# Kernel tuning notes

Measured on AMD Instinct MI355X. Metric: run time of the kernel, lower is better.

The kernel has to match this reference:

```python
import jax, jax.numpy as jnp
import numpy as np

B, T, C = 4, 2048, 1024
N_HEAD = 16


def setup_inputs() -> dict:
    key = jax.random.key(0)
    k1, k2, k3, k4, k5 = jax.random.split(key, 5)
    x = jax.random.normal(k1, (B, T, C), dtype=jnp.float32)
    # c_attn: Dense(3*C) -> kernel [C, 3C], bias [3C]
    w_attn = jax.random.normal(k2, (C, 3 * C), dtype=jnp.float32) * 0.02
    b_attn = jnp.zeros((3 * C,), dtype=jnp.float32)
    # c_proj: Dense(C) with scaled init 0.02/sqrt(2*n_layer), n_layer=24
    w_proj = jax.random.normal(k3, (C, C), dtype=jnp.float32) * (0.02 / np.sqrt(2 * 24))
    b_proj = jnp.zeros((C,), dtype=jnp.float32)
    return {"x": x, "w_attn": w_attn, "b_attn": b_attn, "w_proj": w_proj, "b_proj": b_proj}


def reference(x, w_attn, b_attn, w_proj, b_proj):
    Bx, Tx, Cx = x.shape
    hd = Cx // N_HEAD  # head dim
    qkv = x @ w_attn + b_attn                      # [B, T, 3C]
    q, k, v = jnp.split(qkv, 3, axis=2)
    q = q.reshape(Bx, Tx, N_HEAD, hd).transpose(0, 2, 1, 3)  # [B, H, T, hd]
    k = k.reshape(Bx, Tx, N_HEAD, hd).transpose(0, 2, 1, 3)
    v = v.reshape(Bx, Tx, N_HEAD, hd).transpose(0, 2, 1, 3)
    mask = jnp.tril(jnp.ones((1, 1, Tx, Tx), dtype=bool))
    att = jnp.einsum('bhqd,bhkd->bhqk', q, k) / jnp.sqrt(jnp.float32(hd))
    att = jnp.where(mask, att, jnp.finfo(jnp.float32).min)
    att = jax.nn.softmax(att, axis=-1)
    y = jnp.einsum('bhqk,bhkd->bhqd', att, v)      # [B, H, T, hd]
    y = y.transpose(0, 2, 1, 3).reshape(Bx, Tx, Cx)
    return y @ w_proj + b_proj
```

## Files before the change

### kernel.cpp

```cpp
#include <hip/hip_runtime.h>
#include <cstdint>
#include <cstddef>

typedef unsigned short u16;
typedef __bf16 bf16_t;
typedef bf16_t bf16x8 __attribute__((ext_vector_type(8)));
typedef float f32x4 __attribute__((ext_vector_type(4)));
typedef float f32x16 __attribute__((ext_vector_type(16)));

__device__ __forceinline__ u16 f32_to_bf16(float f) {
  uint32_t u = __builtin_bit_cast(uint32_t, f);
  u += 0x7fffu + ((u >> 16) & 1u);
  return (u16)(u >> 16);
}

__device__ __forceinline__ uint32_t pack_bf16x2(float lo, float hi) {
  uint32_t a = __builtin_bit_cast(uint32_t, hi) + 0x8000u;
  uint32_t b = __builtin_bit_cast(uint32_t, lo) + 0x8000u;
  return __builtin_amdgcn_perm(a, b, 0x07060302u);
}

__device__ __forceinline__ void gload_lds16(const void* g, void* l) {
  __builtin_amdgcn_global_load_lds(
      (const __attribute__((address_space(1))) unsigned int*)g,
      (__attribute__((address_space(3))) unsigned int*)l, 16, 0, 0);
}

__global__ void cvt_bf16(const float* __restrict__ in, u16* __restrict__ out, int n) {
  int i = (blockIdx.x * 256 + threadIdx.x) * 4;
  if (i < n) {
    float4 f = *(const float4*)(in + i);
    ushort4 o;
    o.x = f32_to_bf16(f.x); o.y = f32_to_bf16(f.y);
    o.z = f32_to_bf16(f.z); o.w = f32_to_bf16(f.w);
    *(ushort4*)(out + i) = o;
  }
}

__global__ void tconv(const float* __restrict__ in, u16* __restrict__ out, int R, int C) {
  __shared__ u16 t[64][80];
  int tid = threadIdx.x;
  int cb = blockIdx.x * 64, rb = blockIdx.y * 64;
  int rr = tid >> 2, cg = (tid & 3) * 16;
  const float* ip = in + (size_t)(rb + rr) * C + cb + cg;
#pragma unroll
  for (int i = 0; i < 16; ++i) t[rr][cg + i] = f32_to_bf16(ip[i]);
  __syncthreads();
  int cc = tid >> 2, rg = (tid & 3) * 16;
  u16* op = out + (size_t)(cb + cc) * R + rb + rg;
  union { uint4 v[2]; u16 s[16]; } tmp;
#pragma unroll
  for (int i = 0; i < 16; ++i) tmp.s[i] = t[rg + i][cc];
  *(uint4*)op = tmp.v[0];
  *(uint4*)(op + 8) = tmp.v[1];
}

__global__ void vtrans(const u16* __restrict__ qkvb, u16* __restrict__ vt) {
  __shared__ u16 t[64][80];
  int tid = threadIdx.x;
  int bh = blockIdx.x, tb = blockIdx.y * 64;
  int b = bh >> 4, h = bh & 15;
  int tt = tid >> 2, dg = (tid & 3) * 16;
  const u16* ip = qkvb + (size_t)(b * 2048 + tb + tt) * 3072 + 2048 + h * 64 + dg;
  union { uint4 v; u16 s[8]; } a0, a1;
  a0.v = *(const uint4*)ip;
  a1.v = *(const uint4*)(ip + 8);
#pragma unroll
  for (int i = 0; i < 8; ++i) { t[tt][dg + i] = a0.s[i]; t[tt][dg + 8 + i] = a1.s[i]; }
  __syncthreads();
  int dd = tid >> 2, tg = (tid & 3) * 16;
  u16* op = vt + (size_t)(bh * 64 + dd) * 2048 + tb + tg;
  union { uint4 v[2]; u16 s[16]; } tmp;
#pragma unroll
  for (int i = 0; i < 16; ++i) {
    int pi = (i & 3) | ((i & 4) << 1) | ((i & 8) >> 1);
    tmp.s[i] = t[tg + pi][dd];
  }
  *(uint4*)op = tmp.v[0];
  *(uint4*)(op + 8) = tmp.v[1];
}

template <int OUT_BF16>
__global__ __launch_bounds__(512, 2) void gemm256(const u16* __restrict__ A,
                                                  const u16* __restrict__ Bt,
                                                  const float* __restrict__ bias,
                                                  void* __restrict__ Cout,
                                                  int M, int N, int K) {
  __shared__ __align__(16) u16 lds[2][2][16384];
  const int tid = threadIdx.x;
  const int w = tid >> 6, L = tid & 63;
  const int quad = L >> 4, lc = L & 15;
  const int wr = w >> 2, wc = w & 3;
  const int wrM = wr * 128, wcN = wc * 64;
  const int rL = L >> 3;
  const int gsw = (L & 7) ^ rL;

  const int nbx = N >> 8;
  const int cpx = gridDim.x >> 3;
  const int id = blockIdx.x;
  const int swz = (id & 7) * cpx + (id >> 3);
  const int tileN = (swz % nbx) << 8;
  const int tileM = (swz / nbx) << 8;
  const int nkt = K >> 6;

  u16* const A0 = &lds[0][0][0];
  u16* const B0 = &lds[0][1][0];
  u16* const A1 = &lds[1][0][0];
  u16* const B1 = &lds[1][1][0];

  auto stageQ = [&](const u16* Mp, int gRow, int kt, u16* reg) {
    int ktc = kt < nkt ? kt : nkt - 1;
    const u16* src = Mp + (size_t)(gRow + w * 8 + rL) * K + (ktc << 6) + gsw * 8;
    gload_lds16(src, reg + w * 512);
  };

  f32x4 acc[8][4] = {};
  const int rsw = lc & 7;
  const int g0 = (quad ^ rsw) * 8;
  const int g1 = ((4 + quad) ^ rsw) * 8;
  const int aRow = (wrM + lc) * 64;
  const int bRow = (wcN + lc) * 64;

  stageQ(A, tileM + 0, 0, A0 + 0);
  stageQ(A, tileM + 128, 0, A0 + 8192);
  stageQ(Bt, tileN + 0, 0, B0 + 0);
  stageQ(Bt, tileN + 64, 0, B0 + 4096);
  stageQ(A, tileM + 64, 0, A0 + 4096);
  stageQ(A, tileM + 192, 0, A0 + 12288);
  stageQ(Bt, tileN + 128, 0, B0 + 8192);
  stageQ(Bt, tileN + 192, 0, B0 + 12288);
  stageQ(A, tileM + 0, 1, A1 + 0);
  stageQ(A, tileM + 128, 1, A1 + 8192);
  stageQ(Bt, tileN + 0, 1, B1 + 0);
  stageQ(Bt, tileN + 64, 1, B1 + 4096);
  stageQ(A, tileM + 64, 1, A1 + 4096);
  stageQ(A, tileM + 192, 1, A1 + 12288);
  asm volatile("s_waitcnt vmcnt(6)" ::: "memory");
  __builtin_amdgcn_s_barrier();

  auto group = [&](u16* Ab, u16* Bb, u16* Bob, int T) {
    bf16x8 af[4][2], blo[2][2], bhi[2][2];
#pragma unroll
    for (int mi = 0; mi < 4; ++mi) {
      af[mi][0] = *(const bf16x8*)&Ab[aRow + mi * 1024 + g0];
      af[mi][1] = *(const bf16x8*)&Ab[aRow + mi * 1024 + g1];
    }
#pragma unroll
    for (int ni = 0; ni < 2; ++ni) {
      blo[ni][0] = *(const bf16x8*)&Bb[bRow + ni * 1024 + g0];
      blo[ni][1] = *(const bf16x8*)&Bb[bRow + ni * 1024 + g1];
    }
    stageQ(Bt, tileN + 128, T + 1, Bob + 8192);
    stageQ(Bt, tileN + 192, T + 1, Bob + 12288);
    asm volatile("" ::: "memory");
    __builtin_amdgcn_s_barrier();
    asm volatile("s_waitcnt lgkmcnt(0)" ::: "memory");
    __builtin_amdgcn_s_setprio(1);
#pragma unroll
    for (int mi = 0; mi < 4; ++mi)
#pragma unroll
      for (int ni = 0; ni < 2; ++ni) {
        acc[mi][ni] = __builtin_amdgcn_mfma_f32_16x16x32_bf16(af[mi][0], blo[ni][0], acc[mi][ni], 0, 0, 0);
        acc[mi][ni] = __builtin_amdgcn_mfma_f32_16x16x32_bf16(af[mi][1], blo[ni][1], acc[mi][ni], 0, 0, 0);
      }
    __builtin_amdgcn_s_setprio(0);
    asm volatile("" ::: "memory");
    __builtin_amdgcn_s_barrier();
#pragma unroll
    for (int ni = 0; ni < 2; ++ni) {
      bhi[ni][0] = *(const bf16x8*)&Bb[bRow + (2 + ni) * 1024 + g0];
      bhi[ni][1] = *(const bf16x8*)&Bb[bRow + (2 + ni) * 1024 + g1];
    }
    stageQ(A, tileM + 0, T + 2, Ab + 0);
    stageQ(A, tileM + 128, T + 2, Ab + 8192);
    asm volatile("" ::: "memory");
    __builtin_amdgcn_s_barrier();
    asm volatile("s_waitcnt lgkmcnt(0)" ::: "memory");
    __builtin_amdgcn_s_setprio(1);
#pragma unroll
    for (int mi = 0; mi < 4; ++mi)
#pragma unroll
      for (int ni = 0; ni < 2; ++ni) {
        acc[mi][ni + 2] = __builtin_amdgcn_mfma_f32_16x16x32_bf16(af[mi][0], bhi[ni][0], acc[mi][ni + 2], 0, 0, 0);
        acc[mi][ni + 2] = __builtin_amdgcn_mfma_f32_16x16x32_bf16(af[mi][1], bhi[ni][1], acc[mi][ni + 2], 0, 0, 0);
      }
    __builtin_amdgcn_s_setprio(0);
    asm volatile("" ::: "memory");
    __builtin_amdgcn_s_barrier();
#pragma unroll
    for (int mi = 0; mi < 4; ++mi) {
      af[mi][0] = *(const bf16x8*)&Ab[aRow + (4 + mi) * 1024 + g0];
      af[mi][1] = *(const bf16x8*)&Ab[aRow + (4 + mi) * 1024 + g1];
    }
    stageQ(Bt, tileN + 0, T + 2, Bb + 0);
    stageQ(Bt, tileN + 64, T + 2, Bb + 4096);
    asm volatile("" ::: "memory");
    __builtin_amdgcn_s_barrier();
    asm volatile("s_waitcnt lgkmcnt(0)" ::: "memory");
    __builtin_amdgcn_s_setprio(1);
#pragma unroll
    for (int mi = 0; mi < 4; ++mi)
#pragma unroll
      for (int ni = 0; ni < 2; ++ni) {
        acc[mi + 4][ni + 2] = __builtin_amdgcn_mfma_f32_16x16x32_bf16(af[mi][0], bhi[ni][0], acc[mi + 4][ni + 2], 0, 0, 0);
        acc[mi + 4][ni + 2] = __builtin_amdgcn_mfma_f32_16x16x32_bf16(af[mi][1], bhi[ni][1], acc[mi + 4][ni + 2], 0, 0, 0);
      }
    __builtin_amdgcn_s_setprio(0);
    asm volatile("" ::: "memory");
    __builtin_amdgcn_s_barrier();
    stageQ(A, tileM + 64, T + 2, Ab + 4096);
    stageQ(A, tileM + 192, T + 2, Ab + 12288);
    asm volatile("" ::: "memory");
    __builtin_amdgcn_s_barrier();
    __builtin_amdgcn_s_setprio(1);
#pragma unroll
    for (int mi = 0; mi < 4; ++mi)
#pragma unroll
      for (int ni = 0; ni < 2; ++ni) {
        acc[mi + 4][ni] = __builtin_amdgcn_mfma_f32_16x16x32_bf16(af[mi][0], blo[ni][0], acc[mi + 4][ni], 0, 0, 0);
        acc[mi + 4][ni] = __builtin_amdgcn_mfma_f32_16x16x32_bf16(af[mi][1], blo[ni][1], acc[mi + 4][ni], 0, 0, 0);
      }
    __builtin_amdgcn_s_setprio(0);
    asm volatile("s_waitcnt vmcnt(6)" ::: "memory");
    __builtin_amdgcn_s_barrier();
  };

  for (int T = 0; T < nkt; T += 2) {
    group(A0, B0, B1, T);
    group(A1, B1, B0, T + 1);
  }

  asm volatile("s_waitcnt vmcnt(0)" ::: "memory");

#pragma unroll
  for (int mi = 0; mi < 8; ++mi) {
    int rowb = tileM + wrM + mi * 16 + quad * 4;
#pragma unroll
    for (int ni = 0; ni < 4; ++ni) {
      int col = tileN + wcN + ni * 16 + lc;
      float bv = bias[col];
#pragma unroll
      for (int r = 0; r < 4; ++r) {
        float v = acc[mi][ni][r] + bv;
        if (OUT_BF16)
          ((u16*)Cout)[(size_t)(rowb + r) * N + col] = f32_to_bf16(v);
        else
          ((float*)Cout)[(size_t)(rowb + r) * N + col] = v;
      }
    }
  }
}

__global__ __launch_bounds__(128, 2) void attn(const u16* __restrict__ qkvb,
                                               const u16* __restrict__ vt,
                                               u16* __restrict__ yb) {
  __shared__ __align__(16) u16 kv[2][16][512];
  const int tid = threadIdx.x;
  const int w = tid >> 6, L = tid & 63;
  const int l5 = L & 31, hi = L >> 5;
  const int bh = blockIdx.x;
  const int b = bh >> 4, h = bh & 15;
  const int pair = blockIdx.y;
  const float e_c = 0.18033688f;

  const bool isK = (w == 0);
  const u16* kbase = qkvb + ((size_t)(b * 2048 + l5) * 3072 + 1024 + h * 64 + hi * 8);
  const u16* vbase = vt + ((size_t)(bh * 64 + l5) * 2048 + hi * 8);

  auto stage = [&](int kb2, int buf) {
    if (isK) {
#pragma unroll
      for (int i = 0; i < 8; ++i)
        gload_lds16(kbase + (size_t)(kb2 + (i >> 2) * 32) * 3072 + (i & 3) * 16,
                    &kv[buf][i][0]);
    } else {
#pragma unroll
      for (int i = 0; i < 8; ++i)
        gload_lds16(vbase + (size_t)((i >> 2) * 32) * 2048 + kb2 + (i & 3) * 16,
                    &kv[buf][8 + i][0]);
    }
  };

  int par = 0;
  stage(0, 0);

  for (int pass = 0; pass < 2; ++pass) {
    const int qt = pass ? (31 - pair) : pair;
    const int qbase = qt * 64;
    const int qrow = qbase + w * 32 + l5;
    const int lim = w * 32 + l5 - hi * 4;

    bf16x8 qf[4];
    {
      const u16* qp = qkvb + ((size_t)(b * 2048 + qrow) * 3072 + h * 64 + hi * 8);
#pragma unroll
      for (int ds = 0; ds < 4; ++ds) qf[ds] = *(const bf16x8*)(qp + ds * 16);
    }
    f32x16 o0 = {}, o1 = {};
    float lsum = 0.f;

    for (int kb = 0; kb <= qbase; kb += 64) {
      const bool diag = (kb == qbase);
      __syncthreads();
      stage((kb < qbase) ? kb + 64 : 0, par ^ 1);

      f32x16 st0 = {}, st1 = {};
      __builtin_amdgcn_s_setprio(1);
#pragma unroll
      for (int ds = 0; ds < 4; ++ds) {
        bf16x8 k0 = *(const bf16x8*)&kv[par][ds][L * 8];
        bf16x8 k1 = *(const bf16x8*)&kv[par][4 + ds][L * 8];
        st0 = __builtin_amdgcn_mfma_f32_32x32x16_bf16(k0, qf[ds], st0, 0, 0, 0);
        st1 = __builtin_amdgcn_mfma_f32_32x32x16_bf16(k1, qf[ds], st1, 0, 0, 0);
      }
      __builtin_amdgcn_s_setprio(0);

#pragma unroll
      for (int r = 0; r < 16; ++r) {
        float p0 = __builtin_amdgcn_exp2f(st0[r] * e_c);
        float p1 = __builtin_amdgcn_exp2f(st1[r] * e_c);
        if (diag) {
          const int br = (r & 3) + 8 * (r >> 2);
          p0 = (br <= lim) ? p0 : 0.f;
          p1 = (32 + br <= lim) ? p1 : 0.f;
        }
        st0[r] = p0;
        st1[r] = p1;
        lsum += p0 + p1;
      }

      __builtin_amdgcn_s_setprio(1);
#pragma unroll
      for (int sg = 0; sg < 2; ++sg) {
        union { uint32_t u[4]; bf16x8 v; } pf0, pf1;
#pragma unroll
        for (int q2 = 0; q2 < 4; ++q2) {
          pf0.u[q2] = pack_bf16x2(st0[sg * 8 + q2 * 2], st0[sg * 8 + q2 * 2 + 1]);
          pf1.u[q2] = pack_bf16x2(st1[sg * 8 + q2 * 2], st1[sg * 8 + q2 * 2 + 1]);
        }
        const int ks0 = sg, ks1 = 2 + sg;
        bf16x8 va = *(const bf16x8*)&kv[par][8 + ks0][L * 8];
        bf16x8 vb = *(const bf16x8*)&kv[par][12 + ks0][L * 8];
        o0 = __builtin_amdgcn_mfma_f32_32x32x16_bf16(va, pf0.v, o0, 0, 0, 0);
        o1 = __builtin_amdgcn_mfma_f32_32x32x16_bf16(vb, pf0.v, o1, 0, 0, 0);
        va = *(const bf16x8*)&kv[par][8 + ks1][L * 8];
        vb = *(const bf16x8*)&kv[par][12 + ks1][L * 8];
        o0 = __builtin_amdgcn_mfma_f32_32x32x16_bf16(va, pf1.v, o0, 0, 0, 0);
        o1 = __builtin_amdgcn_mfma_f32_32x32x16_bf16(vb, pf1.v, o1, 0, 0, 0);
      }
      __builtin_amdgcn_s_setprio(0);

      par ^= 1;
    }

    lsum += __shfl_xor(lsum, 32);
    float inv = 1.f / lsum;

    u16* yp = yb + (size_t)(b * 2048 + qrow) * 1024 + h * 64 + hi * 4;
#pragma unroll
    for (int g = 0; g < 4; ++g) {
      uint2 pk;
      pk.x = pack_bf16x2(o0[g * 4 + 0] * inv, o0[g * 4 + 1] * inv);
      pk.y = pack_bf16x2(o0[g * 4 + 2] * inv, o0[g * 4 + 3] * inv);
      *(uint2*)(yp + g * 8) = pk;
      pk.x = pack_bf16x2(o1[g * 4 + 0] * inv, o1[g * 4 + 1] * inv);
      pk.y = pack_bf16x2(o1[g * 4 + 2] * inv, o1[g * 4 + 3] * inv);
      *(uint2*)(yp + 32 + g * 8) = pk;
    }
  }

  asm volatile("s_waitcnt vmcnt(0)" ::: "memory");
}

extern "C" void kernel_launch(void* const* d_in, const int* in_sizes, int n_in,
                              void* d_out, int out_size, void* d_ws, size_t ws_size,
                              hipStream_t stream) {
  const float* x = (const float*)d_in[0];
  const float* w_attn = (const float*)d_in[1];
  const float* b_attn = (const float*)d_in[2];
  const float* w_proj = (const float*)d_in[3];
  const float* b_proj = (const float*)d_in[4];
  float* out = (float*)d_out;

  char* ws = (char*)d_ws;
  u16* xb = (u16*)ws;    ws += (size_t)8192 * 1024 * 2;
  u16* waT = (u16*)ws;   ws += (size_t)3072 * 1024 * 2;
  u16* wpT = (u16*)ws;   ws += (size_t)1024 * 1024 * 2;
  u16* qkvb = (u16*)ws;  ws += (size_t)8192 * 3072 * 2;
  u16* vtb = (u16*)ws;   ws += (size_t)64 * 64 * 2048 * 2;
  u16* yb = (u16*)ws;    ws += (size_t)8192 * 1024 * 2;

  cvt_bf16<<<8192, 256, 0, stream>>>(x, xb, 8192 * 1024);
  tconv<<<dim3(3072 / 64, 1024 / 64), 256, 0, stream>>>(w_attn, waT, 1024, 3072);
  tconv<<<dim3(1024 / 64, 1024 / 64), 256, 0, stream>>>(w_proj, wpT, 1024, 1024);
  gemm256<1><<<dim3(384), 512, 0, stream>>>(xb, waT, b_attn, qkvb, 8192, 3072, 1024);
  vtrans<<<dim3(64, 32), 256, 0, stream>>>(qkvb, vtb);
  attn<<<dim3(64, 16), 128, 0, stream>>>(qkvb, vtb, yb);
  gemm256<0><<<dim3(128), 512, 0, stream>>>(yb, wpT, b_proj, out, 8192, 1024, 1024);
}
```

Before: 273.7 us.

## Split attention into one query tile per block, single-buffered LDS, more occupancy

The attention kernel now launches one block per query tile (32 per head) instead of pairing a short and long tile in each block. K/V staging drops from double-buffered to single-buffered LDS, with a sync before and after each compute step, and launch bounds are raised to allow four blocks per SM. The aim is to get more parallelism and hide latency through occupancy rather than through in-block prefetch. The cost is that global-to-LDS loads are no longer overlapped with MFMA work inside a block, and the causal triangle gives uneven per-block work, which depends on the reversed tile order to balance.

```diff
diff --git a/kernel.cpp b/kernel.cpp
--- a/kernel.cpp
+++ b/kernel.cpp
@@ -251,125 +251,117 @@
   }
 }
 
-__global__ __launch_bounds__(128, 2) void attn(const u16* __restrict__ qkvb,
+__global__ __launch_bounds__(128, 4) void attn(const u16* __restrict__ qkvb,
                                                const u16* __restrict__ vt,
                                                u16* __restrict__ yb) {
-  __shared__ __align__(16) u16 kv[2][16][512];
+  __shared__ __align__(16) u16 kv[16][512];
   const int tid = threadIdx.x;
   const int w = tid >> 6, L = tid & 63;
   const int l5 = L & 31, hi = L >> 5;
   const int bh = blockIdx.x;
   const int b = bh >> 4, h = bh & 15;
-  const int pair = blockIdx.y;
+  const int qt = 31 - blockIdx.y;
   const float e_c = 0.18033688f;
 
   const bool isK = (w == 0);
   const u16* kbase = qkvb + ((size_t)(b * 2048 + l5) * 3072 + 1024 + h * 64 + hi * 8);
   const u16* vbase = vt + ((size_t)(bh * 64 + l5) * 2048 + hi * 8);
 
-  auto stage = [&](int kb2, int buf) {
+  auto stage = [&](int kb2) {
     if (isK) {
 #pragma unroll
       for (int i = 0; i < 8; ++i)
         gload_lds16(kbase + (size_t)(kb2 + (i >> 2) * 32) * 3072 + (i & 3) * 16,
-                    &kv[buf][i][0]);
+                    &kv[i][0]);
     } else {
 #pragma unroll
       for (int i = 0; i < 8; ++i)
         gload_lds16(vbase + (size_t)((i >> 2) * 32) * 2048 + kb2 + (i & 3) * 16,
-                    &kv[buf][8 + i][0]);
+                    &kv[8 + i][0]);
     }
   };
 
-  int par = 0;
-  stage(0, 0);
-
-  for (int pass = 0; pass < 2; ++pass) {
-    const int qt = pass ? (31 - pair) : pair;
-    const int qbase = qt * 64;
-    const int qrow = qbase + w * 32 + l5;
-    const int lim = w * 32 + l5 - hi * 4;
-
-    bf16x8 qf[4];
-    {
-      const u16* qp = qkvb + ((size_t)(b * 2048 + qrow) * 3072 + h * 64 + hi * 8);
-#pragma unroll
-      for (int ds = 0; ds < 4; ++ds) qf[ds] = *(const bf16x8*)(qp + ds * 16);
-    }
-    f32x16 o0 = {}, o1 = {};
-    float lsum = 0.f;
-
-    for (int kb = 0; kb <= qbase; kb += 64) {
-      const bool diag = (kb == qbase);
-      __syncthreads();
-      stage((kb < qbase) ? kb + 64 : 0, par ^ 1);
-
-      f32x16 st0 = {}, st1 = {};
-      __builtin_amdgcn_s_setprio(1);
-#pragma unroll
-      for (int ds = 0; ds < 4; ++ds) {
-        bf16x8 k0 = *(const bf16x8*)&kv[par][ds][L * 8];
-        bf16x8 k1 = *(const bf16x8*)&kv[par][4 + ds][L * 8];
-        st0 = __builtin_amdgcn_mfma_f32_32x32x16_bf16(k0, qf[ds], st0, 0, 0, 0);
-        st1 = __builtin_amdgcn_mfma_f32_32x32x16_bf16(k1, qf[ds], st1, 0, 0, 0);
-      }
-      __builtin_amdgcn_s_setprio(0);
-
-#pragma unroll
-      for (int r = 0; r < 16; ++r) {
-        float p0 = __builtin_amdgcn_exp2f(st0[r] * e_c);
-        float p1 = __builtin_amdgcn_exp2f(st1[r] * e_c);
-        if (diag) {
-          const int br = (r & 3) + 8 * (r >> 2);
-          p0 = (br <= lim) ? p0 : 0.f;
-          p1 = (32 + br <= lim) ? p1 : 0.f;
-        }
-        st0[r] = p0;
-        st1[r] = p1;
-        lsum += p0 + p1;
-      }
-
-      __builtin_amdgcn_s_setprio(1);
-#pragma unroll
-      for (int sg = 0; sg < 2; ++sg) {
-        union { uint32_t u[4]; bf16x8 v; } pf0, pf1;
-#pragma unroll
-        for (int q2 = 0; q2 < 4; ++q2) {
-          pf0.u[q2] = pack_bf16x2(st0[sg * 8 + q2 * 2], st0[sg * 8 + q2 * 2 + 1]);
-          pf1.u[q2] = pack_bf16x2(st1[sg * 8 + q2 * 2], st1[sg * 8 + q2 * 2 + 1]);
-        }
-        const int ks0 = sg, ks1 = 2 + sg;
-        bf16x8 va = *(const bf16x8*)&kv[par][8 + ks0][L * 8];
-        bf16x8 vb = *(const bf16x8*)&kv[par][12 + ks0][L * 8];
-        o0 = __builtin_amdgcn_mfma_f32_32x32x16_bf16(va, pf0.v, o0, 0, 0, 0);
-        o1 = __builtin_amdgcn_mfma_f32_32x32x16_bf16(vb, pf0.v, o1, 0, 0, 0);
-        va = *(const bf16x8*)&kv[par][8 + ks1][L * 8];
-        vb = *(const bf16x8*)&kv[par][12 + ks1][L * 8];
-        o0 = __builtin_amdgcn_mfma_f32_32x32x16_bf16(va, pf1.v, o0, 0, 0, 0);
-        o1 = __builtin_amdgcn_mfma_f32_32x32x16_bf16(vb, pf1.v, o1, 0, 0, 0);
-      }
-      __builtin_amdgcn_s_setprio(0);
-
-      par ^= 1;
-    }
-
-    lsum += __shfl_xor(lsum, 32);
-    float inv = 1.f / lsum;
-
-    u16* yp = yb + (size_t)(b * 2048 + qrow) * 1024 + h * 64 + hi * 4;
-#pragma unroll
-    for (int g = 0; g < 4; ++g) {
-      uint2 pk;
-      pk.x = pack_bf16x2(o0[g * 4 + 0] * inv, o0[g * 4 + 1] * inv);
-      pk.y = pack_bf16x2(o0[g * 4 + 2] * inv, o0[g * 4 + 3] * inv);
-      *(uint2*)(yp + g * 8) = pk;
-      pk.x = pack_bf16x2(o1[g * 4 + 0] * inv, o1[g * 4 + 1] * inv);
-      pk.y = pack_bf16x2(o1[g * 4 + 2] * inv, o1[g * 4 + 3] * inv);
-      *(uint2*)(yp + 32 + g * 8) = pk;
-    }
-  }
-
-  asm volatile("s_waitcnt vmcnt(0)" ::: "memory");
+  const int qbase = qt * 64;
+  const int qrow = qbase + w * 32 + l5;
+  const int lim = w * 32 + l5 - hi * 4;
+
+  bf16x8 qf[4];
+  {
+    const u16* qp = qkvb + ((size_t)(b * 2048 + qrow) * 3072 + h * 64 + hi * 8);
+#pragma unroll
+    for (int ds = 0; ds < 4; ++ds) qf[ds] = *(const bf16x8*)(qp + ds * 16);
+  }
+  f32x16 o0 = {}, o1 = {};
+  float lsum = 0.f;
+
+  for (int kb = 0; kb <= qbase; kb += 64) {
+    const bool diag = (kb == qbase);
+    stage(kb);
+    __syncthreads();
+
+    f32x16 st0 = {}, st1 = {};
+    __builtin_amdgcn_s_setprio(1);
+#pragma unroll
+    for (int ds = 0; ds < 4; ++ds) {
+      bf16x8 k0 = *(const bf16x8*)&kv[ds][L * 8];
+      bf16x8 k1 = *(const bf16x8*)&kv[4 + ds][L * 8];
+      st0 = __builtin_amdgcn_mfma_f32_32x32x16_bf16(k0, qf[ds], st0, 0, 0, 0);
+      st1 = __builtin_amdgcn_mfma_f32_32x32x16_bf16(k1, qf[ds], st1, 0, 0, 0);
+    }
+    __builtin_amdgcn_s_setprio(0);
+
+#pragma unroll
+    for (int r = 0; r < 16; ++r) {
+      float p0 = __builtin_amdgcn_exp2f(st0[r] * e_c);
+      float p1 = __builtin_amdgcn_exp2f(st1[r] * e_c);
+      if (diag) {
+        const int br = (r & 3) + 8 * (r >> 2);
+        p0 = (br <= lim) ? p0 : 0.f;
+        p1 = (32 + br <= lim) ? p1 : 0.f;
+      }
+      st0[r] = p0;
+      st1[r] = p1;
+      lsum += p0 + p1;
+    }
+
+    __builtin_amdgcn_s_setprio(1);
+#pragma unroll
+    for (int sg = 0; sg < 2; ++sg) {
+      union { uint32_t u[4]; bf16x8 v; } pf0, pf1;
+#pragma unroll
+      for (int q2 = 0; q2 < 4; ++q2) {
+        pf0.u[q2] = pack_bf16x2(st0[sg * 8 + q2 * 2], st0[sg * 8 + q2 * 2 + 1]);
+        pf1.u[q2] = pack_bf16x2(st1[sg * 8 + q2 * 2], st1[sg * 8 + q2 * 2 + 1]);
+      }
+      const int ks0 = sg, ks1 = 2 + sg;
+      bf16x8 va = *(const bf16x8*)&kv[8 + ks0][L * 8];
+      bf16x8 vb = *(const bf16x8*)&kv[12 + ks0][L * 8];
+      o0 = __builtin_amdgcn_mfma_f32_32x32x16_bf16(va, pf0.v, o0, 0, 0, 0);
+      o1 = __builtin_amdgcn_mfma_f32_32x32x16_bf16(vb, pf0.v, o1, 0, 0, 0);
+      va = *(const bf16x8*)&kv[8 + ks1][L * 8];
+      vb = *(const bf16x8*)&kv[12 + ks1][L * 8];
+      o0 = __builtin_amdgcn_mfma_f32_32x32x16_bf16(va, pf1.v, o0, 0, 0, 0);
+      o1 = __builtin_amdgcn_mfma_f32_32x32x16_bf16(vb, pf1.v, o1, 0, 0, 0);
+    }
+    __builtin_amdgcn_s_setprio(0);
+
+    __syncthreads();
+  }
+
+  lsum += __shfl_xor(lsum, 32);
+  float inv = 1.f / lsum;
+
+  u16* yp = yb + (size_t)(b * 2048 + qrow) * 1024 + h * 64 + hi * 4;
+#pragma unroll
+  for (int g = 0; g < 4; ++g) {
+    uint2 pk;
+    pk.x = pack_bf16x2(o0[g * 4 + 0] * inv, o0[g * 4 + 1] * inv);
+    pk.y = pack_bf16x2(o0[g * 4 + 2] * inv, o0[g * 4 + 3] * inv);
+    *(uint2*)(yp + g * 8) = pk;
+    pk.x = pack_bf16x2(o1[g * 4 + 0] * inv, o1[g * 4 + 1] * inv);
+    pk.y = pack_bf16x2(o1[g * 4 + 2] * inv, o1[g * 4 + 3] * inv);
+    *(uint2*)(yp + 32 + g * 8) = pk;
+  }
 }
 
 extern "C" void kernel_launch(void* const* d_in, const int* in_sizes, int n_in,
@@ -395,6 +387,6 @@
   tconv<<<dim3(1024 / 64, 1024 / 64), 256, 0, stream>>>(w_proj, wpT, 1024, 1024);
   gemm256<1><<<dim3(384), 512, 0, stream>>>(xb, waT, b_attn, qkvb, 8192, 3072, 1024);
   vtrans<<<dim3(64, 32), 256, 0, stream>>>(qkvb, vtb);
-  attn<<<dim3(64, 16), 128, 0, stream>>>(qkvb, vtb, yb);
+  attn<<<dim3(64, 32), 128, 0, stream>>>(qkvb, vtb, yb);
   gemm256<0><<<dim3(128), 512, 0, stream>>>(yb, wpT, b_proj, out, 8192, 1024, 1024);
 }
```

New measurement: 280.4 us. 1.02x slower.

## Use 8-wave attention blocks sharing K/V tiles across 256 query rows

Applied to the files above, without the earlier changes.

The attention kernel moves from 2-wave blocks that each handle a pair of 64-row query tiles to 8-wave blocks that each own a 256-row query tile. All eight waves split the K/V staging and reuse each staged 64-key tile, so a tile loaded into LDS now serves four times as many queries. Causal masking now skips whole key tiles per wave, and only partially masked tiles get the per-element mask. The trade-off is that waves whose queries are already finished still wait at the barriers while later waves compute, and grid-level load balance is coarser with fewer, larger blocks.

```diff
diff --git a/kernel.cpp b/kernel.cpp
--- a/kernel.cpp
+++ b/kernel.cpp
@@ -251,7 +251,7 @@
   }
 }
 
-__global__ __launch_bounds__(128, 2) void attn(const u16* __restrict__ qkvb,
+__global__ __launch_bounds__(512, 4) void attn(const u16* __restrict__ qkvb,
                                                const u16* __restrict__ vt,
                                                u16* __restrict__ yb) {
   __shared__ __align__(16) u16 kv[2][16][512];
@@ -260,49 +260,50 @@
   const int l5 = L & 31, hi = L >> 5;
   const int bh = blockIdx.x;
   const int b = bh >> 4, h = bh & 15;
-  const int pair = blockIdx.y;
+  const int qt = (blockIdx.y < 4) ? (7 - blockIdx.y) : (blockIdx.y - 4);
   const float e_c = 0.18033688f;
-
-  const bool isK = (w == 0);
-  const u16* kbase = qkvb + ((size_t)(b * 2048 + l5) * 3072 + 1024 + h * 64 + hi * 8);
-  const u16* vbase = vt + ((size_t)(bh * 64 + l5) * 2048 + hi * 8);
+  const int qbase = qt * 256;
+  const int wq = qbase + w * 32;
+  const int nk = qbase + 256;
+
+  const int u = w - 4;
+  const u16* kb0 = qkvb + (size_t)(b * 2048 + (w >> 1) * 32 + l5) * 3072 + 1024 +
+                   h * 64 + (w & 1) * 32 + hi * 8;
+  const u16* vb0 = vt + (size_t)(bh * 64 + (u >> 1) * 32 + l5) * 2048 +
+                   (u & 1) * 32 + hi * 8;
 
   auto stage = [&](int kb2, int buf) {
-    if (isK) {
-#pragma unroll
-      for (int i = 0; i < 8; ++i)
-        gload_lds16(kbase + (size_t)(kb2 + (i >> 2) * 32) * 3072 + (i & 3) * 16,
-                    &kv[buf][i][0]);
+    if (w < 4) {
+      const u16* s = kb0 + (size_t)kb2 * 3072;
+      gload_lds16(s, &kv[buf][2 * w][0]);
+      gload_lds16(s + 16, &kv[buf][2 * w + 1][0]);
     } else {
-#pragma unroll
-      for (int i = 0; i < 8; ++i)
-        gload_lds16(vbase + (size_t)((i >> 2) * 32) * 2048 + kb2 + (i & 3) * 16,
-                    &kv[buf][8 + i][0]);
+      const u16* s = vb0 + kb2;
+      gload_lds16(s, &kv[buf][8 + 2 * u][0]);
+      gload_lds16(s + 16, &kv[buf][8 + 2 * u + 1][0]);
     }
   };
+
+  const int qrow = wq + l5;
+  bf16x8 qf[4];
+  {
+    const u16* qp = qkvb + ((size_t)(b * 2048 + qrow) * 3072 + h * 64 + hi * 8);
+#pragma unroll
+    for (int ds = 0; ds < 4; ++ds) qf[ds] = *(const bf16x8*)(qp + ds * 16);
+  }
+  f32x16 o0 = {}, o1 = {};
+  float lsum = 0.f;
 
   int par = 0;
   stage(0, 0);
 
-  for (int pass = 0; pass < 2; ++pass) {
-    const int qt = pass ? (31 - pair) : pair;
-    const int qbase = qt * 64;
-    const int qrow = qbase + w * 32 + l5;
-    const int lim = w * 32 + l5 - hi * 4;
-
-    bf16x8 qf[4];
-    {
-      const u16* qp = qkvb + ((size_t)(b * 2048 + qrow) * 3072 + h * 64 + hi * 8);
-#pragma unroll
-      for (int ds = 0; ds < 4; ++ds) qf[ds] = *(const bf16x8*)(qp + ds * 16);
-    }
-    f32x16 o0 = {}, o1 = {};
-    float lsum = 0.f;
-
-    for (int kb = 0; kb <= qbase; kb += 64) {
-      const bool diag = (kb == qbase);
-      __syncthreads();
-      stage((kb < qbase) ? kb + 64 : 0, par ^ 1);
+  for (int kb = 0; kb < nk; kb += 64) {
+    __syncthreads();
+    stage((kb + 64 < nk) ? kb + 64 : 0, par ^ 1);
+
+    if (kb <= wq + 31) {
+      const bool part = (kb + 63 > wq);
+      const int lim = qrow - 4 * hi - kb;
 
       f32x16 st0 = {}, st1 = {};
       __builtin_amdgcn_s_setprio(1);
@@ -319,7 +320,7 @@
       for (int r = 0; r < 16; ++r) {
         float p0 = __builtin_amdgcn_exp2f(st0[r] * e_c);
         float p1 = __builtin_amdgcn_exp2f(st1[r] * e_c);
-        if (diag) {
+        if (part) {
           const int br = (r & 3) + 8 * (r >> 2);
           p0 = (br <= lim) ? p0 : 0.f;
           p1 = (32 + br <= lim) ? p1 : 0.f;
@@ -349,24 +350,24 @@
         o1 = __builtin_amdgcn_mfma_f32_32x32x16_bf16(vb, pf1.v, o1, 0, 0, 0);
       }
       __builtin_amdgcn_s_setprio(0);
-
-      par ^= 1;
-    }
-
-    lsum += __shfl_xor(lsum, 32);
-    float inv = 1.f / lsum;
-
-    u16* yp = yb + (size_t)(b * 2048 + qrow) * 1024 + h * 64 + hi * 4;
-#pragma unroll
-    for (int g = 0; g < 4; ++g) {
-      uint2 pk;
-      pk.x = pack_bf16x2(o0[g * 4 + 0] * inv, o0[g * 4 + 1] * inv);
-      pk.y = pack_bf16x2(o0[g * 4 + 2] * inv, o0[g * 4 + 3] * inv);
-      *(uint2*)(yp + g * 8) = pk;
-      pk.x = pack_bf16x2(o1[g * 4 + 0] * inv, o1[g * 4 + 1] * inv);
-      pk.y = pack_bf16x2(o1[g * 4 + 2] * inv, o1[g * 4 + 3] * inv);
-      *(uint2*)(yp + 32 + g * 8) = pk;
-    }
+    }
+
+    par ^= 1;
+  }
+
+  lsum += __shfl_xor(lsum, 32);
+  float inv = 1.f / lsum;
+
+  u16* yp = yb + (size_t)(b * 2048 + qrow) * 1024 + h * 64 + hi * 4;
+#pragma unroll
+  for (int g = 0; g < 4; ++g) {
+    uint2 pk;
+    pk.x = pack_bf16x2(o0[g * 4 + 0] * inv, o0[g * 4 + 1] * inv);
+    pk.y = pack_bf16x2(o0[g * 4 + 2] * inv, o0[g * 4 + 3] * inv);
+    *(uint2*)(yp + g * 8) = pk;
+    pk.x = pack_bf16x2(o1[g * 4 + 0] * inv, o1[g * 4 + 1] * inv);
+    pk.y = pack_bf16x2(o1[g * 4 + 2] * inv, o1[g * 4 + 3] * inv);
+    *(uint2*)(yp + 32 + g * 8) = pk;
   }
 
   asm volatile("s_waitcnt vmcnt(0)" ::: "memory");
@@ -395,6 +396,6 @@
   tconv<<<dim3(1024 / 64, 1024 / 64), 256, 0, stream>>>(w_proj, wpT, 1024, 1024);
   gemm256<1><<<dim3(384), 512, 0, stream>>>(xb, waT, b_attn, qkvb, 8192, 3072, 1024);
   vtrans<<<dim3(64, 32), 256, 0, stream>>>(qkvb, vtb);
-  attn<<<dim3(64, 16), 128, 0, stream>>>(qkvb, vtb, yb);
+  attn<<<dim3(64, 8), 512, 0, stream>>>(qkvb, vtb, yb);
   gemm256<0><<<dim3(128), 512, 0, stream>>>(yb, wpT, b_proj, out, 8192, 1024, 1024);
 }
```

Measured after the change: 258.0 us. 1.06x faster.
